# Kernel optimization log

Measured on AMD Instinct MI355X. Metric: run time of the kernel, lower is better.

## Reference

```python
import jax, jax.numpy as jnp
import numpy as np

B, T, C, HS = 4, 512, 128, 64

def setup_inputs() -> dict:
    key = jax.random.key(0)
    ks = jax.random.split(key, 8)
    s1 = 1.0 / np.sqrt(2 * C)  # torch Linear default init scale ~ U(-1/sqrt(in),1/sqrt(in))
    s2 = 1.0 / np.sqrt(C)
    return {
        "x": jax.random.normal(ks[0], (B, T, C), jnp.float32),
        "pos_emb": jax.random.normal(ks[1], (T, C), jnp.float32),
        # att2 layer 1: Linear(2C -> C); stored as [2C, C] (in, out)
        "W1": jax.random.uniform(ks[2], (2 * C, C), jnp.float32, -s1, s1),
        "b1": jax.random.uniform(ks[3], (C,), jnp.float32, -s1, s1),
        # att2 layer 2: Linear(C -> 1)
        "W2": jax.random.uniform(ks[4], (C, 1), jnp.float32, -s2, s2),
        "b2": jax.random.uniform(ks[5], (1,), jnp.float32, -s2, s2),
        # value: Linear(C -> HS, bias=False)
        "Wv": jax.random.uniform(ks[6], (C, HS), jnp.float32, -s2, s2),
    }


def reference(x, pos_emb, W1, b1, W2, b2, Wv):
    b, t, c = x.shape
    x1 = pos_emb + x  # [b,t,c]
    # Pairwise feature: cat([x1[j], x1[i]], -1) at position [i, j].
    # First Linear on the concat splits into two [c,c] blocks -> avoids
    # materializing the [b,t,t,2c] concat while computing identical math.
    W1k, W1q = W1[:c], W1[c:]            # rows for k-part (x1[j]) and q-part (x1[i])
    Ak = jnp.einsum('bjc,cd->bjd', x1, W1k)  # [b,t,c] contribution from key index j
    Aq = jnp.einsum('bic,cd->bid', x1, W1q)  # [b,t,c] contribution from query index i
    hidden = jax.nn.relu(Aq[:, :, None, :] + Ak[:, None, :, :] + b1)  # [b,t,t,c]
    wei = (jnp.einsum('bijc,co->bijo', hidden, W2)[..., 0] + b2[0]) * (c ** -0.5)  # [b,t,t]
    # causal mask (tril)
    mask = jnp.tril(jnp.ones((t, t), dtype=bool))
    wei = jnp.where(mask, wei, -jnp.inf)
    wei = jax.nn.softmax(wei, axis=-1)
    v = jnp.einsum('btc,ch->bth', x, Wv)  # [b,t,hs]
    out = jnp.einsum('bij,bjh->bih', wei, v)
    return out
```

## Files before the change

### kernel.cpp

```cpp
#include <hip/hip_runtime.h>
#include <math.h>

#define B_ 4
#define T_ 512
#define C_ 128
#define HS_ 64

typedef float f4 __attribute__((ext_vector_type(4)));
typedef float f2 __attribute__((ext_vector_type(2)));

#define SCALE_ 0.08838834764831845f

static __device__ __forceinline__ f2 relu2(f2 v) {
    v.x = fmaxf(v.x, 0.f);
    v.y = fmaxf(v.y, 0.f);
    return v;
}

__global__ __launch_bounds__(640) void k_prep(
    const float* __restrict__ x, const float* __restrict__ pos,
    const float* __restrict__ W1, const float* __restrict__ b1,
    const float* __restrict__ Wv,
    float* __restrict__ Aq, float* __restrict__ AkT, float* __restrict__ V)
{
    __shared__ float x1s[8 * 132];
    __shared__ float xs[8 * 132];
    const int t = threadIdx.x;
    const int row0 = blockIdx.x * 8;

    if (t < 256) {
        int r = t >> 5, cq = t & 31;
        int gr = row0 + r;
        f4 xv = *(const f4*)(x + gr * 128 + cq * 4);
        f4 pv = *(const f4*)(pos + (gr & 511) * 128 + cq * 4);
        *(f4*)&xs[r * 132 + cq * 4] = xv;
        *(f4*)&x1s[r * 132 + cq * 4] = xv + pv;
    }
    __syncthreads();

    const int q = t >> 3;
    const int r = t & 7;

    const float* wbase;
    int wstr, col0;
    const float* xb;
    f4 binit = {0.f, 0.f, 0.f, 0.f};
    if (q < 32) {
        col0 = q * 4;
        wbase = W1 + 128 * 128 + col0;
        wstr = 128;
        xb = x1s;
        binit = *(const f4*)(b1 + col0);
    } else if (q < 64) {
        col0 = (q - 32) * 4;
        wbase = W1 + col0;
        wstr = 128;
        xb = x1s;
    } else {
        col0 = (q - 64) * 4;
        wbase = Wv + col0;
        wstr = 64;
        xb = xs;
    }

    f4 acc = binit;
    const float* xr = xb + r * 132;
#pragma unroll 8
    for (int c = 0; c < 128; ++c) {
        f4 w = *(const f4*)(wbase + c * wstr);
        acc += xr[c] * w;
    }

    const int gr = row0 + r;
    if (q < 32) {
        *(f4*)(Aq + (size_t)gr * 128 + col0) = acc;
    } else if (q < 64) {
        const int bb = gr >> 9, j = gr & 511;
        float* base = AkT + ((size_t)bb * 128 + col0) * 512 + j;
        base[0]    = acc.x;
        base[512]  = acc.y;
        base[1024] = acc.z;
        base[1536] = acc.w;
    } else {
        *(f4*)(V + (size_t)gr * 64 + col0) = acc;
    }
}

__global__ __launch_bounds__(256) void k_fused(
    const float* __restrict__ Aq, const float* __restrict__ AkT,
    const float* __restrict__ V, const float* __restrict__ W2,
    float* __restrict__ out)
{
    __shared__ float pbuf[4][2][128];
    __shared__ float accs[4][2][64];
    __shared__ float mls[4][2][2];

    const int t = threadIdx.x;
    const int w = t >> 6;
    const int lane = t & 63;
    const int bx = blockIdx.x;
    const int b = bx & 3;
    const int g = 255 - (bx >> 2);
    const int r0 = g * 2, r1 = g * 2 + 1;

    const int j0 = w * 128 + lane * 2;

    float m0 = -1e30f, m1 = -1e30f, l0 = 0.f, l1 = 0.f;
    float a0 = 0.f, a1 = 0.f;

    if (w * 128 <= r1) {
        const bool act0 = (w * 128 <= r0);

        const float* aq0 = Aq + (size_t)(b * T_ + r0) * C_;
        const float* aq1 = aq0 + C_;
        const float* akt = AkT + (size_t)b * C_ * T_ + j0;
        f2 s0a = {0.f, 0.f}, s0b = {0.f, 0.f};
        f2 s1a = {0.f, 0.f}, s1b = {0.f, 0.f};
#pragma unroll 4
        for (int c = 0; c < 128; c += 2) {
            f2 k0 = *(const f2*)(akt + (size_t)c * 512);
            f2 k1 = *(const f2*)(akt + (size_t)(c + 1) * 512);
            const float q00 = aq0[c], q01 = aq0[c + 1];
            const float q10 = aq1[c], q11 = aq1[c + 1];
            const float w0 = W2[c], w1 = W2[c + 1];
            s0a += relu2(k0 + q00) * w0;
            s0b += relu2(k1 + q01) * w1;
            s1a += relu2(k0 + q10) * w0;
            s1b += relu2(k1 + q11) * w1;
        }
        const f2 s0 = (s0a + s0b) * SCALE_;
        const f2 s1 = (s1a + s1b) * SCALE_;

        const float s00 = (j0     <= r0) ? s0.x : -1e30f;
        const float s01 = (j0 + 1 <= r0) ? s0.y : -1e30f;
        const float s10 = (j0     <= r1) ? s1.x : -1e30f;
        const float s11 = (j0 + 1 <= r1) ? s1.y : -1e30f;

        float t0 = fmaxf(s00, s01), t1 = fmaxf(s10, s11);
#pragma unroll
        for (int off = 1; off < 64; off <<= 1) {
            t0 = fmaxf(t0, __shfl_xor(t0, off));
            t1 = fmaxf(t1, __shfl_xor(t1, off));
        }
        const float p00 = act0 ? __expf(s00 - t0) : 0.f;
        const float p01 = act0 ? __expf(s01 - t0) : 0.f;
        const float p10 = __expf(s10 - t1);
        const float p11 = __expf(s11 - t1);
        m0 = act0 ? t0 : -1e30f;
        m1 = t1;

        pbuf[w][0][lane * 2]     = p00;
        pbuf[w][0][lane * 2 + 1] = p01;
        pbuf[w][1][lane * 2]     = p10;
        pbuf[w][1][lane * 2 + 1] = p11;

        float ls0 = p00 + p01, ls1 = p10 + p11;
#pragma unroll
        for (int off = 1; off < 64; off <<= 1) {
            ls0 += __shfl_xor(ls0, off);
            ls1 += __shfl_xor(ls1, off);
        }
        l0 = ls0;
        l1 = ls1;

        const float* vt = V + (size_t)b * T_ * HS_ + (size_t)(w * 128) * HS_ + lane;
        float a0e = 0.f, a0o = 0.f, a1e = 0.f, a1o = 0.f;
#pragma unroll 4
        for (int q8 = 0; q8 < 32; ++q8) {
            f4 p0 = *(const f4*)&pbuf[w][0][q8 * 4];
            f4 p1 = *(const f4*)&pbuf[w][1][q8 * 4];
            const float v0 = vt[(q8 * 4 + 0) * HS_];
            const float v1 = vt[(q8 * 4 + 1) * HS_];
            const float v2 = vt[(q8 * 4 + 2) * HS_];
            const float v3 = vt[(q8 * 4 + 3) * HS_];
            a0e += p0.x * v0 + p0.z * v2;
            a0o += p0.y * v1 + p0.w * v3;
            a1e += p1.x * v0 + p1.z * v2;
            a1o += p1.y * v1 + p1.w * v3;
        }
        a0 = a0e + a0o;
        a1 = a1e + a1o;
    }

    accs[w][0][lane] = a0;
    accs[w][1][lane] = a1;
    if (lane == 0) {
        mls[w][0][0] = m0; mls[w][0][1] = l0;
        mls[w][1][0] = m1; mls[w][1][1] = l1;
    }
    __syncthreads();

    if (w < 2) {
        const int r = w ? r1 : r0;
        const float ma = mls[0][w][0], mb = mls[1][w][0];
        const float mc = mls[2][w][0], md = mls[3][w][0];
        const float ms = fmaxf(fmaxf(ma, mb), fmaxf(mc, md));
        const float ea = __expf(ma - ms), eb = __expf(mb - ms);
        const float ec = __expf(mc - ms), ed = __expf(md - ms);
        const float num = accs[0][w][lane] * ea + accs[1][w][lane] * eb +
                          accs[2][w][lane] * ec + accs[3][w][lane] * ed;
        const float den = mls[0][w][1] * ea + mls[1][w][1] * eb +
                          mls[2][w][1] * ec + mls[3][w][1] * ed;
        out[(size_t)(b * T_ + r) * HS_ + lane] = num / den;
    }
}

extern "C" void kernel_launch(void* const* d_in, const int* in_sizes, int n_in,
                              void* d_out, int out_size, void* d_ws, size_t ws_size,
                              hipStream_t stream)
{
    const float* x   = (const float*)d_in[0];
    const float* pos = (const float*)d_in[1];
    const float* W1  = (const float*)d_in[2];
    const float* b1  = (const float*)d_in[3];
    const float* W2  = (const float*)d_in[4];
    const float* b2  = (const float*)d_in[5];  (void)b2;
    const float* Wv  = (const float*)d_in[6];
    float* out = (float*)d_out;
    float* ws = (float*)d_ws;

    float* Aq  = ws;
    float* AkT = ws + 262144;
    float* V   = ws + 524288;

    k_prep<<<dim3(256), dim3(640), 0, stream>>>(x, pos, W1, b1, Wv, Aq, AkT, V);
    k_fused<<<dim3(1024), dim3(256), 0, stream>>>(Aq, AkT, V, W2, out);
}
```

Measured before the change: 33.71 us.

## Tile pairwise scores into 16-row × 64-key LDS blocks with split-K merge kernel

Replaces the per-row-pair fused kernel with a kernel that stages a 64-key AkT slice and 16 query rows in shared memory and computes 4 rows per wave. Only causal (lower-triangle) tiles are launched, indexed with a triangular mapping. Each tile writes partial softmax max, sum and weighted-V results to workspace, and a third kernel merges them. This raises reuse of key and query data from shared memory instead of global loads. The cost is an extra launch, a global round trip for the partials, and more workspace.

Measured after the change: 39.49 us. +17.1%, slower.

```diff
diff --git a/kernel.cpp b/kernel.cpp
--- a/kernel.cpp
+++ b/kernel.cpp
@@ -7,15 +7,8 @@
 #define HS_ 64
 
 typedef float f4 __attribute__((ext_vector_type(4)));
-typedef float f2 __attribute__((ext_vector_type(2)));
 
 #define SCALE_ 0.08838834764831845f
-
-static __device__ __forceinline__ f2 relu2(f2 v) {
-    v.x = fmaxf(v.x, 0.f);
-    v.y = fmaxf(v.y, 0.f);
-    return v;
-}
 
 __global__ __launch_bounds__(640) void k_prep(
     const float* __restrict__ x, const float* __restrict__ pos,
@@ -86,123 +79,151 @@
     }
 }
 
-__global__ __launch_bounds__(256) void k_fused(
+__global__ __launch_bounds__(256) void k_fusedp(
     const float* __restrict__ Aq, const float* __restrict__ AkT,
     const float* __restrict__ V, const float* __restrict__ W2,
-    float* __restrict__ out)
-{
-    __shared__ float pbuf[4][2][128];
-    __shared__ float accs[4][2][64];
-    __shared__ float mls[4][2][2];
+    float* __restrict__ pml, float* __restrict__ pacc)
+{
+    __shared__ float aks[128][64];
+    __shared__ float aqs[16][128];
+    __shared__ float w2s[128];
+    __shared__ float pbuf[4][4][64];
 
     const int t = threadIdx.x;
-    const int w = t >> 6;
+    const int b = blockIdx.y;
+    const int f = blockIdx.x;
+
+    int n = (int)((1.0f + sqrtf(1.0f + 2.0f * (float)f)) * 0.5f);
+    while (2 * n * (n - 1) > f) --n;
+    while (2 * n * (n + 1) <= f) ++n;
+    const int rem = f - 2 * n * (n - 1);
+    const int G = 4 * (n - 1) + rem / n;
+    const int w = rem % n;
+    const int j0 = w * 64;
+    const int row0 = G * 16;
+
+    const float* aktw = AkT + (size_t)b * 128 * 512 + j0;
+    for (int idx = t; idx < 2048; idx += 256) {
+        int c = idx >> 4, qq = idx & 15;
+        *(f4*)&aks[c][qq * 4] = *(const f4*)(aktw + (size_t)c * 512 + qq * 4);
+    }
+    const float* aqg = Aq + (size_t)(b * 512 + row0) * 128;
+    for (int idx = t; idx < 512; idx += 256) {
+        int r = idx >> 5, cq = idx & 31;
+        *(f4*)&aqs[r][cq * 4] = *(const f4*)(aqg + r * 128 + cq * 4);
+    }
+    if (t < 32) *(f4*)&w2s[t * 4] = *(const f4*)(W2 + t * 4);
+    __syncthreads();
+
+    const int w8 = t >> 6;
     const int lane = t & 63;
-    const int bx = blockIdx.x;
-    const int b = bx & 3;
-    const int g = 255 - (bx >> 2);
-    const int r0 = g * 2, r1 = g * 2 + 1;
-
-    const int j0 = w * 128 + lane * 2;
-
-    float m0 = -1e30f, m1 = -1e30f, l0 = 0.f, l1 = 0.f;
-    float a0 = 0.f, a1 = 0.f;
-
-    if (w * 128 <= r1) {
-        const bool act0 = (w * 128 <= r0);
-
-        const float* aq0 = Aq + (size_t)(b * T_ + r0) * C_;
-        const float* aq1 = aq0 + C_;
-        const float* akt = AkT + (size_t)b * C_ * T_ + j0;
-        f2 s0a = {0.f, 0.f}, s0b = {0.f, 0.f};
-        f2 s1a = {0.f, 0.f}, s1b = {0.f, 0.f};
+    const int rb = 4 * w8;
+    const int r0 = row0 + rb, r1 = r0 + 1, r2 = r0 + 2, r3 = r0 + 3;
+    const int gj = j0 + lane;
+
+    float m0 = -1e30f, m1 = -1e30f, m2 = -1e30f, m3 = -1e30f;
+    float l0 = 0.f, l1 = 0.f, l2 = 0.f, l3 = 0.f;
+    float a0 = 0.f, a1 = 0.f, a2 = 0.f, a3 = 0.f;
+
+    if (r3 >= j0) {
+        float s0 = 0.f, s1 = 0.f, s2 = 0.f, s3 = 0.f;
 #pragma unroll 4
-        for (int c = 0; c < 128; c += 2) {
-            f2 k0 = *(const f2*)(akt + (size_t)c * 512);
-            f2 k1 = *(const f2*)(akt + (size_t)(c + 1) * 512);
-            const float q00 = aq0[c], q01 = aq0[c + 1];
-            const float q10 = aq1[c], q11 = aq1[c + 1];
-            const float w0 = W2[c], w1 = W2[c + 1];
-            s0a += relu2(k0 + q00) * w0;
-            s0b += relu2(k1 + q01) * w1;
-            s1a += relu2(k0 + q10) * w0;
-            s1b += relu2(k1 + q11) * w1;
-        }
-        const f2 s0 = (s0a + s0b) * SCALE_;
-        const f2 s1 = (s1a + s1b) * SCALE_;
-
-        const float s00 = (j0     <= r0) ? s0.x : -1e30f;
-        const float s01 = (j0 + 1 <= r0) ? s0.y : -1e30f;
-        const float s10 = (j0     <= r1) ? s1.x : -1e30f;
-        const float s11 = (j0 + 1 <= r1) ? s1.y : -1e30f;
-
-        float t0 = fmaxf(s00, s01), t1 = fmaxf(s10, s11);
+        for (int c = 0; c < 128; ++c) {
+            const float ak = aks[c][lane];
+            const float wv = w2s[c];
+            s0 += fmaxf(ak + aqs[rb + 0][c], 0.f) * wv;
+            s1 += fmaxf(ak + aqs[rb + 1][c], 0.f) * wv;
+            s2 += fmaxf(ak + aqs[rb + 2][c], 0.f) * wv;
+            s3 += fmaxf(ak + aqs[rb + 3][c], 0.f) * wv;
+        }
+        s0 = (gj <= r0) ? s0 * SCALE_ : -1e30f;
+        s1 = (gj <= r1) ? s1 * SCALE_ : -1e30f;
+        s2 = (gj <= r2) ? s2 * SCALE_ : -1e30f;
+        s3 = (gj <= r3) ? s3 * SCALE_ : -1e30f;
+
+        float t0 = s0, t1 = s1, t2 = s2, t3 = s3;
 #pragma unroll
         for (int off = 1; off < 64; off <<= 1) {
             t0 = fmaxf(t0, __shfl_xor(t0, off));
             t1 = fmaxf(t1, __shfl_xor(t1, off));
-        }
-        const float p00 = act0 ? __expf(s00 - t0) : 0.f;
-        const float p01 = act0 ? __expf(s01 - t0) : 0.f;
-        const float p10 = __expf(s10 - t1);
-        const float p11 = __expf(s11 - t1);
-        m0 = act0 ? t0 : -1e30f;
-        m1 = t1;
-
-        pbuf[w][0][lane * 2]     = p00;
-        pbuf[w][0][lane * 2 + 1] = p01;
-        pbuf[w][1][lane * 2]     = p10;
-        pbuf[w][1][lane * 2 + 1] = p11;
-
-        float ls0 = p00 + p01, ls1 = p10 + p11;
+            t2 = fmaxf(t2, __shfl_xor(t2, off));
+            t3 = fmaxf(t3, __shfl_xor(t3, off));
+        }
+        const float p0 = __expf(s0 - t0);
+        const float p1 = __expf(s1 - t1);
+        const float p2 = __expf(s2 - t2);
+        const float p3 = __expf(s3 - t3);
+        pbuf[w8][0][lane] = p0;
+        pbuf[w8][1][lane] = p1;
+        pbuf[w8][2][lane] = p2;
+        pbuf[w8][3][lane] = p3;
+        float u0 = p0, u1 = p1, u2 = p2, u3 = p3;
 #pragma unroll
         for (int off = 1; off < 64; off <<= 1) {
-            ls0 += __shfl_xor(ls0, off);
-            ls1 += __shfl_xor(ls1, off);
-        }
-        l0 = ls0;
-        l1 = ls1;
-
-        const float* vt = V + (size_t)b * T_ * HS_ + (size_t)(w * 128) * HS_ + lane;
-        float a0e = 0.f, a0o = 0.f, a1e = 0.f, a1o = 0.f;
+            u0 += __shfl_xor(u0, off);
+            u1 += __shfl_xor(u1, off);
+            u2 += __shfl_xor(u2, off);
+            u3 += __shfl_xor(u3, off);
+        }
+
+        const float* vt = V + ((size_t)b * 512 + j0) * 64 + lane;
+        float b0 = 0.f, b1v = 0.f, b2v = 0.f, b3 = 0.f;
 #pragma unroll 4
-        for (int q8 = 0; q8 < 32; ++q8) {
-            f4 p0 = *(const f4*)&pbuf[w][0][q8 * 4];
-            f4 p1 = *(const f4*)&pbuf[w][1][q8 * 4];
-            const float v0 = vt[(q8 * 4 + 0) * HS_];
-            const float v1 = vt[(q8 * 4 + 1) * HS_];
-            const float v2 = vt[(q8 * 4 + 2) * HS_];
-            const float v3 = vt[(q8 * 4 + 3) * HS_];
-            a0e += p0.x * v0 + p0.z * v2;
-            a0o += p0.y * v1 + p0.w * v3;
-            a1e += p1.x * v0 + p1.z * v2;
-            a1o += p1.y * v1 + p1.w * v3;
-        }
-        a0 = a0e + a0o;
-        a1 = a1e + a1o;
-    }
-
-    accs[w][0][lane] = a0;
-    accs[w][1][lane] = a1;
+        for (int q4 = 0; q4 < 16; ++q4) {
+            f4 q0 = *(const f4*)&pbuf[w8][0][q4 * 4];
+            f4 q1 = *(const f4*)&pbuf[w8][1][q4 * 4];
+            f4 q2 = *(const f4*)&pbuf[w8][2][q4 * 4];
+            f4 q3 = *(const f4*)&pbuf[w8][3][q4 * 4];
+            const float v0 = vt[(q4 * 4 + 0) * 64];
+            const float v1 = vt[(q4 * 4 + 1) * 64];
+            const float v2 = vt[(q4 * 4 + 2) * 64];
+            const float v3 = vt[(q4 * 4 + 3) * 64];
+            b0  += q0.x * v0 + q0.y * v1 + q0.z * v2 + q0.w * v3;
+            b1v += q1.x * v0 + q1.y * v1 + q1.z * v2 + q1.w * v3;
+            b2v += q2.x * v0 + q2.y * v1 + q2.z * v2 + q2.w * v3;
+            b3  += q3.x * v0 + q3.y * v1 + q3.z * v2 + q3.w * v3;
+        }
+
+        const bool c0 = (r0 >= j0), c1 = (r1 >= j0), c2 = (r2 >= j0);
+        m0 = c0 ? t0 : -1e30f;  l0 = c0 ? u0 : 0.f;  a0 = c0 ? b0 : 0.f;
+        m1 = c1 ? t1 : -1e30f;  l1 = c1 ? u1 : 0.f;  a1 = c1 ? b1v : 0.f;
+        m2 = c2 ? t2 : -1e30f;  l2 = c2 ? u2 : 0.f;  a2 = c2 ? b2v : 0.f;
+        m3 = t3;                l3 = u3;             a3 = b3;
+    }
+
+    const size_t k0 = ((size_t)(b * 512 + r0) * 8 + w);
+    pacc[(k0 + 0 ) * 64 + lane] = a0;
+    pacc[(k0 + 8 ) * 64 + lane] = a1;
+    pacc[(k0 + 16) * 64 + lane] = a2;
+    pacc[(k0 + 24) * 64 + lane] = a3;
     if (lane == 0) {
-        mls[w][0][0] = m0; mls[w][0][1] = l0;
-        mls[w][1][0] = m1; mls[w][1][1] = l1;
-    }
-    __syncthreads();
-
-    if (w < 2) {
-        const int r = w ? r1 : r0;
-        const float ma = mls[0][w][0], mb = mls[1][w][0];
-        const float mc = mls[2][w][0], md = mls[3][w][0];
-        const float ms = fmaxf(fmaxf(ma, mb), fmaxf(mc, md));
-        const float ea = __expf(ma - ms), eb = __expf(mb - ms);
-        const float ec = __expf(mc - ms), ed = __expf(md - ms);
-        const float num = accs[0][w][lane] * ea + accs[1][w][lane] * eb +
-                          accs[2][w][lane] * ec + accs[3][w][lane] * ed;
-        const float den = mls[0][w][1] * ea + mls[1][w][1] * eb +
-                          mls[2][w][1] * ec + mls[3][w][1] * ed;
-        out[(size_t)(b * T_ + r) * HS_ + lane] = num / den;
-    }
+        pml[(k0 + 0 ) * 2] = m0;  pml[(k0 + 0 ) * 2 + 1] = l0;
+        pml[(k0 + 8 ) * 2] = m1;  pml[(k0 + 8 ) * 2 + 1] = l1;
+        pml[(k0 + 16) * 2] = m2;  pml[(k0 + 16) * 2 + 1] = l2;
+        pml[(k0 + 24) * 2] = m3;  pml[(k0 + 24) * 2 + 1] = l3;
+    }
+}
+
+__global__ __launch_bounds__(256) void k_merge(
+    const float* __restrict__ pml, const float* __restrict__ pacc,
+    float* __restrict__ out)
+{
+    const int t = threadIdx.x;
+    const int w8 = t >> 6, lane = t & 63;
+    const int grow = blockIdx.x * 4 + w8;
+    const int i = grow & 511;
+    const int nw = (i >> 6) + 1;
+    const size_t base = (size_t)grow * 8;
+
+    float ms = -1e30f;
+    for (int w = 0; w < nw; ++w) ms = fmaxf(ms, pml[(base + w) * 2]);
+    float num = 0.f, den = 0.f;
+    for (int w = 0; w < nw; ++w) {
+        const float e = __expf(pml[(base + w) * 2] - ms);
+        den += pml[(base + w) * 2 + 1] * e;
+        num += pacc[(base + w) * 64 + lane] * e;
+    }
+    out[(size_t)grow * 64 + lane] = num / den;
 }
 
 extern "C" void kernel_launch(void* const* d_in, const int* in_sizes, int n_in,
@@ -219,10 +240,13 @@
     float* out = (float*)d_out;
     float* ws = (float*)d_ws;
 
-    float* Aq  = ws;
-    float* AkT = ws + 262144;
-    float* V   = ws + 524288;
+    float* Aq   = ws;
+    float* AkT  = ws + 262144;
+    float* V    = ws + 524288;
+    float* pml  = ws + 655360;
+    float* pacc = ws + 688128;
 
     k_prep<<<dim3(256), dim3(640), 0, stream>>>(x, pos, W1, b1, Wv, Aq, AkT, V);
-    k_fused<<<dim3(1024), dim3(256), 0, stream>>>(Aq, AkT, V, W2, out);
-}
+    k_fusedp<<<dim3(144, B_), dim3(256), 0, stream>>>(Aq, AkT, V, W2, pml, pacc);
+    k_merge<<<dim3(512), dim3(256), 0, stream>>>(pml, pacc, out);
+}
```

## Fuse projection and attention into one cooperative kernel with grid sync

Applied to the files above, without the earlier changes.

Merges the projection kernel and the fused attention kernel into a single cooperative launch of 512 blocks, with a grid-wide sync between the two phases. Each block now handles 4 query rows instead of 2, so every loaded AkT and V element is reused across more rows. The final per-row combine now involves all four waves instead of two. This removes one kernel launch and the gap between kernels, at the cost of grid-sync overhead, higher register pressure, and halving the number of blocks in the attention phase.

Measured after the change: 94.90 us. 2.81x slower.

```diff
diff --git a/kernel.cpp b/kernel.cpp
--- a/kernel.cpp
+++ b/kernel.cpp
@@ -1,5 +1,8 @@
 #include <hip/hip_runtime.h>
+#include <hip/hip_cooperative_groups.h>
 #include <math.h>
+
+namespace cg = cooperative_groups;
 
 #define B_ 4
 #define T_ 512
@@ -17,192 +20,166 @@
     return v;
 }
 
-__global__ __launch_bounds__(640) void k_prep(
+__global__ __launch_bounds__(256, 2) void k_all(
     const float* __restrict__ x, const float* __restrict__ pos,
     const float* __restrict__ W1, const float* __restrict__ b1,
-    const float* __restrict__ Wv,
-    float* __restrict__ Aq, float* __restrict__ AkT, float* __restrict__ V)
-{
-    __shared__ float x1s[8 * 132];
-    __shared__ float xs[8 * 132];
-    const int t = threadIdx.x;
-    const int row0 = blockIdx.x * 8;
-
-    if (t < 256) {
-        int r = t >> 5, cq = t & 31;
-        int gr = row0 + r;
-        f4 xv = *(const f4*)(x + gr * 128 + cq * 4);
-        f4 pv = *(const f4*)(pos + (gr & 511) * 128 + cq * 4);
-        *(f4*)&xs[r * 132 + cq * 4] = xv;
-        *(f4*)&x1s[r * 132 + cq * 4] = xv + pv;
-    }
-    __syncthreads();
-
-    const int q = t >> 3;
-    const int r = t & 7;
-
-    const float* wbase;
-    int wstr, col0;
-    const float* xb;
-    f4 binit = {0.f, 0.f, 0.f, 0.f};
-    if (q < 32) {
-        col0 = q * 4;
-        wbase = W1 + 128 * 128 + col0;
-        wstr = 128;
-        xb = x1s;
-        binit = *(const f4*)(b1 + col0);
-    } else if (q < 64) {
-        col0 = (q - 32) * 4;
-        wbase = W1 + col0;
-        wstr = 128;
-        xb = x1s;
-    } else {
-        col0 = (q - 64) * 4;
-        wbase = Wv + col0;
-        wstr = 64;
-        xb = xs;
-    }
-
-    f4 acc = binit;
-    const float* xr = xb + r * 132;
-#pragma unroll 8
-    for (int c = 0; c < 128; ++c) {
-        f4 w = *(const f4*)(wbase + c * wstr);
-        acc += xr[c] * w;
-    }
-
-    const int gr = row0 + r;
-    if (q < 32) {
-        *(f4*)(Aq + (size_t)gr * 128 + col0) = acc;
-    } else if (q < 64) {
-        const int bb = gr >> 9, j = gr & 511;
-        float* base = AkT + ((size_t)bb * 128 + col0) * 512 + j;
-        base[0]    = acc.x;
-        base[512]  = acc.y;
-        base[1024] = acc.z;
-        base[1536] = acc.w;
-    } else {
-        *(f4*)(V + (size_t)gr * 64 + col0) = acc;
-    }
-}
-
-__global__ __launch_bounds__(256) void k_fused(
-    const float* __restrict__ Aq, const float* __restrict__ AkT,
-    const float* __restrict__ V, const float* __restrict__ W2,
+    const float* __restrict__ W2, const float* __restrict__ Wv,
+    float* __restrict__ Aq, float* __restrict__ AkT, float* __restrict__ Vv,
     float* __restrict__ out)
 {
-    __shared__ float pbuf[4][2][128];
-    __shared__ float accs[4][2][64];
-    __shared__ float mls[4][2][2];
+    __shared__ float x1s[4][132];
+    __shared__ float xs[4][132];
+    __shared__ float pbuf[4][4][128];
+    __shared__ float accs[4][4][64];
+    __shared__ float mls[4][4][2];
 
     const int t = threadIdx.x;
-    const int w = t >> 6;
-    const int lane = t & 63;
     const int bx = blockIdx.x;
+
+    {
+        const int prow0 = bx * 4;
+        if (t < 128) {
+            const int r = t >> 5, cq = t & 31;
+            const int gr = prow0 + r;
+            f4 xv = *(const f4*)(x + (size_t)gr * 128 + cq * 4);
+            f4 pv = *(const f4*)(pos + (size_t)(gr & 511) * 128 + cq * 4);
+            *(f4*)&xs[r][cq * 4] = xv;
+            *(f4*)&x1s[r][cq * 4] = xv + pv;
+        }
+        __syncthreads();
+
+        for (int u = t; u < 320; u += 256) {
+            const int q = u >> 2, r = u & 3;
+            const int gr = prow0 + r;
+            const float* wbase; int wstr, col0; const float* xb;
+            f4 acc = {0.f, 0.f, 0.f, 0.f};
+            if (q < 32) {
+                col0 = q * 4; wbase = W1 + 16384 + col0; wstr = 128; xb = x1s[r];
+                acc = *(const f4*)(b1 + col0);
+            } else if (q < 64) {
+                col0 = (q - 32) * 4; wbase = W1 + col0; wstr = 128; xb = x1s[r];
+            } else {
+                col0 = (q - 64) * 4; wbase = Wv + col0; wstr = 64; xb = xs[r];
+            }
+#pragma unroll 8
+            for (int c = 0; c < 128; ++c)
+                acc += xb[c] * *(const f4*)(wbase + c * wstr);
+
+            if (q < 32) {
+                *(f4*)(Aq + (size_t)gr * 128 + col0) = acc;
+            } else if (q < 64) {
+                const int bb = gr >> 9, j = gr & 511;
+                float* base = AkT + ((size_t)bb * 128 + col0) * 512 + j;
+                base[0] = acc.x; base[512] = acc.y;
+                base[1024] = acc.z; base[1536] = acc.w;
+            } else {
+                *(f4*)(Vv + (size_t)gr * 64 + col0) = acc;
+            }
+        }
+    }
+
+    cg::this_grid().sync();
+
     const int b = bx & 3;
-    const int g = 255 - (bx >> 2);
-    const int r0 = g * 2, r1 = g * 2 + 1;
-
-    const int j0 = w * 128 + lane * 2;
-
-    float m0 = -1e30f, m1 = -1e30f, l0 = 0.f, l1 = 0.f;
-    float a0 = 0.f, a1 = 0.f;
-
-    if (w * 128 <= r1) {
-        const bool act0 = (w * 128 <= r0);
-
-        const float* aq0 = Aq + (size_t)(b * T_ + r0) * C_;
-        const float* aq1 = aq0 + C_;
-        const float* akt = AkT + (size_t)b * C_ * T_ + j0;
-        f2 s0a = {0.f, 0.f}, s0b = {0.f, 0.f};
-        f2 s1a = {0.f, 0.f}, s1b = {0.f, 0.f};
+    const int g = 127 - (bx >> 2);
+    const int r0 = g * 4;
+    const int w = t >> 6, lane = t & 63;
+    const int j0 = w * 128;
+    const int jA = j0 + lane * 2;
+
+    float m0 = -1e30f, m1 = -1e30f, m2 = -1e30f, m3 = -1e30f;
+    float l0 = 0.f, l1 = 0.f, l2 = 0.f, l3 = 0.f;
+    float a0 = 0.f, a1 = 0.f, a2 = 0.f, a3 = 0.f;
+
+    if (j0 <= r0 + 3) {
+        const float* aq0 = Aq + (size_t)(b * 512 + r0) * 128;
+        const float* aq1 = aq0 + 128;
+        const float* aq2 = aq1 + 128;
+        const float* aq3 = aq2 + 128;
+        const float* akt = AkT + (size_t)b * 65536 + jA;
+
+        f2 s0a = {0,0}, s0b = {0,0}, s1a = {0,0}, s1b = {0,0};
+        f2 s2a = {0,0}, s2b = {0,0}, s3a = {0,0}, s3b = {0,0};
 #pragma unroll 4
         for (int c = 0; c < 128; c += 2) {
-            f2 k0 = *(const f2*)(akt + (size_t)c * 512);
-            f2 k1 = *(const f2*)(akt + (size_t)(c + 1) * 512);
-            const float q00 = aq0[c], q01 = aq0[c + 1];
-            const float q10 = aq1[c], q11 = aq1[c + 1];
+            const f2 k0 = *(const f2*)(akt + (size_t)c * 512);
+            const f2 k1 = *(const f2*)(akt + (size_t)(c + 1) * 512);
             const float w0 = W2[c], w1 = W2[c + 1];
-            s0a += relu2(k0 + q00) * w0;
-            s0b += relu2(k1 + q01) * w1;
-            s1a += relu2(k0 + q10) * w0;
-            s1b += relu2(k1 + q11) * w1;
-        }
-        const f2 s0 = (s0a + s0b) * SCALE_;
-        const f2 s1 = (s1a + s1b) * SCALE_;
-
-        const float s00 = (j0     <= r0) ? s0.x : -1e30f;
-        const float s01 = (j0 + 1 <= r0) ? s0.y : -1e30f;
-        const float s10 = (j0     <= r1) ? s1.x : -1e30f;
-        const float s11 = (j0 + 1 <= r1) ? s1.y : -1e30f;
-
-        float t0 = fmaxf(s00, s01), t1 = fmaxf(s10, s11);
-#pragma unroll
-        for (int off = 1; off < 64; off <<= 1) {
-            t0 = fmaxf(t0, __shfl_xor(t0, off));
-            t1 = fmaxf(t1, __shfl_xor(t1, off));
-        }
-        const float p00 = act0 ? __expf(s00 - t0) : 0.f;
-        const float p01 = act0 ? __expf(s01 - t0) : 0.f;
-        const float p10 = __expf(s10 - t1);
-        const float p11 = __expf(s11 - t1);
-        m0 = act0 ? t0 : -1e30f;
-        m1 = t1;
-
-        pbuf[w][0][lane * 2]     = p00;
-        pbuf[w][0][lane * 2 + 1] = p01;
-        pbuf[w][1][lane * 2]     = p10;
-        pbuf[w][1][lane * 2 + 1] = p11;
-
-        float ls0 = p00 + p01, ls1 = p10 + p11;
-#pragma unroll
-        for (int off = 1; off < 64; off <<= 1) {
-            ls0 += __shfl_xor(ls0, off);
-            ls1 += __shfl_xor(ls1, off);
-        }
-        l0 = ls0;
-        l1 = ls1;
-
-        const float* vt = V + (size_t)b * T_ * HS_ + (size_t)(w * 128) * HS_ + lane;
-        float a0e = 0.f, a0o = 0.f, a1e = 0.f, a1o = 0.f;
+            s0a += relu2(k0 + aq0[c]) * w0;  s0b += relu2(k1 + aq0[c + 1]) * w1;
+            s1a += relu2(k0 + aq1[c]) * w0;  s1b += relu2(k1 + aq1[c + 1]) * w1;
+            s2a += relu2(k0 + aq2[c]) * w0;  s2b += relu2(k1 + aq2[c + 1]) * w1;
+            s3a += relu2(k0 + aq3[c]) * w0;  s3b += relu2(k1 + aq3[c + 1]) * w1;
+        }
+
+#define FINROW(R, SA, SB, MD, LD)                                        \
+        {                                                                \
+            const int rr_ = r0 + (R);                                    \
+            f2 sv = (SA + SB) * SCALE_;                                  \
+            float sx = (jA     <= rr_) ? sv.x : -1e30f;                  \
+            float sy = (jA + 1 <= rr_) ? sv.y : -1e30f;                  \
+            float mx = fmaxf(sx, sy);                                    \
+            _Pragma("unroll")                                            \
+            for (int off = 1; off < 64; off <<= 1)                       \
+                mx = fmaxf(mx, __shfl_xor(mx, off));                     \
+            const bool live_ = (j0 <= rr_);                              \
+            const float px = live_ ? __expf(sx - mx) : 0.f;              \
+            const float py = live_ ? __expf(sy - mx) : 0.f;              \
+            f2 pp = {px, py};                                            \
+            *(f2*)&pbuf[w][R][lane * 2] = pp;                            \
+            float ls = px + py;                                          \
+            _Pragma("unroll")                                            \
+            for (int off = 1; off < 64; off <<= 1)                       \
+                ls += __shfl_xor(ls, off);                               \
+            MD = live_ ? mx : -1e30f;                                    \
+            LD = ls;                                                     \
+        }
+        FINROW(0, s0a, s0b, m0, l0)
+        FINROW(1, s1a, s1b, m1, l1)
+        FINROW(2, s2a, s2b, m2, l2)
+        FINROW(3, s3a, s3b, m3, l3)
+#undef FINROW
+
+        const float* vt = Vv + ((size_t)b * 512 + j0) * 64 + lane;
 #pragma unroll 4
-        for (int q8 = 0; q8 < 32; ++q8) {
-            f4 p0 = *(const f4*)&pbuf[w][0][q8 * 4];
-            f4 p1 = *(const f4*)&pbuf[w][1][q8 * 4];
-            const float v0 = vt[(q8 * 4 + 0) * HS_];
-            const float v1 = vt[(q8 * 4 + 1) * HS_];
-            const float v2 = vt[(q8 * 4 + 2) * HS_];
-            const float v3 = vt[(q8 * 4 + 3) * HS_];
-            a0e += p0.x * v0 + p0.z * v2;
-            a0o += p0.y * v1 + p0.w * v3;
-            a1e += p1.x * v0 + p1.z * v2;
-            a1o += p1.y * v1 + p1.w * v3;
-        }
-        a0 = a0e + a0o;
-        a1 = a1e + a1o;
+        for (int q4 = 0; q4 < 32; ++q4) {
+            const f4 p0 = *(const f4*)&pbuf[w][0][q4 * 4];
+            const f4 p1 = *(const f4*)&pbuf[w][1][q4 * 4];
+            const f4 p2 = *(const f4*)&pbuf[w][2][q4 * 4];
+            const f4 p3 = *(const f4*)&pbuf[w][3][q4 * 4];
+            const float v0 = vt[(q4 * 4 + 0) * 64];
+            const float v1 = vt[(q4 * 4 + 1) * 64];
+            const float v2 = vt[(q4 * 4 + 2) * 64];
+            const float v3 = vt[(q4 * 4 + 3) * 64];
+            a0 += p0.x * v0 + p0.y * v1 + p0.z * v2 + p0.w * v3;
+            a1 += p1.x * v0 + p1.y * v1 + p1.z * v2 + p1.w * v3;
+            a2 += p2.x * v0 + p2.y * v1 + p2.z * v2 + p2.w * v3;
+            a3 += p3.x * v0 + p3.y * v1 + p3.z * v2 + p3.w * v3;
+        }
     }
 
     accs[w][0][lane] = a0;
     accs[w][1][lane] = a1;
+    accs[w][2][lane] = a2;
+    accs[w][3][lane] = a3;
     if (lane == 0) {
         mls[w][0][0] = m0; mls[w][0][1] = l0;
         mls[w][1][0] = m1; mls[w][1][1] = l1;
+        mls[w][2][0] = m2; mls[w][2][1] = l2;
+        mls[w][3][0] = m3; mls[w][3][1] = l3;
     }
     __syncthreads();
 
-    if (w < 2) {
-        const int r = w ? r1 : r0;
-        const float ma = mls[0][w][0], mb = mls[1][w][0];
-        const float mc = mls[2][w][0], md = mls[3][w][0];
-        const float ms = fmaxf(fmaxf(ma, mb), fmaxf(mc, md));
-        const float ea = __expf(ma - ms), eb = __expf(mb - ms);
-        const float ec = __expf(mc - ms), ed = __expf(md - ms);
-        const float num = accs[0][w][lane] * ea + accs[1][w][lane] * eb +
-                          accs[2][w][lane] * ec + accs[3][w][lane] * ed;
-        const float den = mls[0][w][1] * ea + mls[1][w][1] * eb +
-                          mls[2][w][1] * ec + mls[3][w][1] * ed;
-        out[(size_t)(b * T_ + r) * HS_ + lane] = num / den;
-    }
+    const int rr = r0 + w;
+    const int nw = (rr >> 7) + 1;
+    float ms = -1e30f;
+    for (int ww = 0; ww < nw; ++ww) ms = fmaxf(ms, mls[ww][w][0]);
+    float num = 0.f, den = 0.f;
+    for (int ww = 0; ww < nw; ++ww) {
+        const float e = __expf(mls[ww][w][0] - ms);
+        den += mls[ww][w][1] * e;
+        num += accs[ww][w][lane] * e;
+    }
+    out[(size_t)(b * 512 + rr) * 64 + lane] = num / den;
 }
 
 extern "C" void kernel_launch(void* const* d_in, const int* in_sizes, int n_in,
@@ -223,6 +200,9 @@
     float* AkT = ws + 262144;
     float* V   = ws + 524288;
 
-    k_prep<<<dim3(256), dim3(640), 0, stream>>>(x, pos, W1, b1, Wv, Aq, AkT, V);
-    k_fused<<<dim3(1024), dim3(256), 0, stream>>>(Aq, AkT, V, W2, out);
+    void* args[] = {(void*)&x, (void*)&pos, (void*)&W1, (void*)&b1,
+                    (void*)&W2, (void*)&Wv, (void*)&Aq, (void*)&AkT,
+                    (void*)&V, (void*)&out};
+    hipLaunchCooperativeKernel((const void*)k_all, dim3(512), dim3(256),
+                               args, 0, stream);
 }
```
